# Kernel optimization log

Hardware: AMD Instinct MI355X
Metric: run time of the kernel (lower is better)

The kernel has to match this reference:

```python
import jax, jax.numpy as jnp
import numpy as np

N = 100000       # n nodes
NFEAT = 128
NHID1 = 128
NHID2 = 64
NCLASS = 8
E = 1_600_000    # edges per graph (avg degree 16)
HATT = 16        # Attention hidden_size default


def _glorot(k, shape):
    lim = jnp.sqrt(6.0 / (shape[0] + shape[1]))
    return jax.random.uniform(k, shape, minval=-lim, maxval=lim, dtype=jnp.float32)


def setup_inputs() -> dict:
    key = jax.random.key(0)
    ks = jax.random.split(key, 32)
    inp = {}
    inp["x"] = jax.random.normal(ks[0], (N, NFEAT), dtype=jnp.float32)
    inp["sadj_row"] = jax.random.randint(ks[1], (E,), 0, N)
    inp["sadj_col"] = jax.random.randint(ks[2], (E,), 0, N)
    inp["sadj_val"] = jax.random.uniform(ks[3], (E,), dtype=jnp.float32) / 16.0
    inp["fadj_row"] = jax.random.randint(ks[4], (E,), 0, N)
    inp["fadj_col"] = jax.random.randint(ks[5], (E,), 0, N)
    inp["fadj_val"] = jax.random.uniform(ks[6], (E,), dtype=jnp.float32) / 16.0
    # GCN weights: gc1 (nfeat->nhid1), gc2 (nhid1->nhid2), each with bias
    names = ["s1", "s2", "c"]
    for i, nm in enumerate(names):
        inp[f"w_{nm}_1"] = _glorot(ks[7 + 4 * i], (NFEAT, NHID1))
        inp[f"b_{nm}_1"] = jnp.zeros((NHID1,), jnp.float32)
        inp[f"w_{nm}_2"] = _glorot(ks[8 + 4 * i], (NHID1, NHID2))
        inp[f"b_{nm}_2"] = jnp.zeros((NHID2,), jnp.float32)
    # Attention: Linear(nhid2, 16) + Tanh + Linear(16, 1, bias=False)
    inp["att_w1"] = _glorot(ks[20], (NHID2, HATT))
    inp["att_b1"] = jnp.zeros((HATT,), jnp.float32)
    inp["att_w2"] = _glorot(ks[21], (HATT, 1))
    # MLP: Linear(nhid2, nclass)
    inp["mlp_w"] = _glorot(ks[22], (NHID2, NCLASS))
    inp["mlp_b"] = jnp.zeros((NCLASS,), jnp.float32)
    return inp


def _spmm(row, col, val, h):
    # (sparse adj) @ h : out[i] = sum_{edges (i,j)} val * h[j]
    return jax.ops.segment_sum(val[:, None] * h[col], row, num_segments=N)


def _gcn(x, row, col, val, w1, b1, w2, b2):
    h = jax.nn.relu(_spmm(row, col, val, x @ w1) + b1)  # dropout is identity (eval)
    return _spmm(row, col, val, h @ w2) + b2


def reference(x, sadj_row, sadj_col, sadj_val, fadj_row, fadj_col, fadj_val,
              w_s1_1, b_s1_1, w_s1_2, b_s1_2,
              w_s2_1, b_s2_1, w_s2_2, b_s2_2,
              w_c_1, b_c_1, w_c_2, b_c_2,
              att_w1, att_b1, att_w2, mlp_w, mlp_b):
    emb1 = _gcn(x, sadj_row, sadj_col, sadj_val, w_s1_1, b_s1_1, w_s1_2, b_s1_2)
    com1 = _gcn(x, sadj_row, sadj_col, sadj_val, w_c_1, b_c_1, w_c_2, b_c_2)
    com2 = _gcn(x, fadj_row, fadj_col, fadj_val, w_c_1, b_c_1, w_c_2, b_c_2)
    emb2 = _gcn(x, fadj_row, fadj_col, fadj_val, w_s2_1, b_s2_1, w_s2_2, b_s2_2)
    xcom = (com1 + com2) * 0.5
    z = jnp.stack([emb1, emb2, xcom], axis=1)          # [N, 3, nhid2]
    w = jnp.tanh(z @ att_w1 + att_b1) @ att_w2          # [N, 3, 1]
    beta = jax.nn.softmax(w, axis=1)
    emb = (beta * z).sum(axis=1)                        # [N, nhid2]
    output = jax.nn.log_softmax(emb @ mlp_w + mlp_b, axis=1)
    return (output, beta, emb1, com1, com2, emb2, emb)
```

## Files before the change

### kernel.cpp

```cpp
#include <hip/hip_runtime.h>


typedef unsigned short ushort_t;
typedef float f32x4 __attribute__((ext_vector_type(4)));
typedef short short8 __attribute__((ext_vector_type(8)));

#define NBLK1 512

__device__ __forceinline__ ushort_t f2bf(float f) {
  unsigned u = __float_as_uint(f);
  unsigned r = (u + 0x7FFFu + ((u >> 16) & 1u)) >> 16;
  return (ushort_t)r;
}
__device__ __forceinline__ float bf2f(ushort_t b) {
  return __uint_as_float((unsigned)b << 16);
}

__device__ __forceinline__ float rs16(const float a[16], int lane) {
  bool b8 = (lane & 8) != 0;
  float t[8];
#pragma unroll
  for (int j = 0; j < 8; ++j) {
    float sent = b8 ? a[j] : a[j + 8];
    float mine = b8 ? a[j + 8] : a[j];
    t[j] = mine + __shfl_xor(sent, 8);
  }
  bool b4 = (lane & 4) != 0;
  float u[4];
#pragma unroll
  for (int j = 0; j < 4; ++j) {
    float sent = b4 ? t[j] : t[j + 4];
    float mine = b4 ? t[j + 4] : t[j];
    u[j] = mine + __shfl_xor(sent, 4);
  }
  bool b2 = (lane & 2) != 0;
  float v[2];
#pragma unroll
  for (int j = 0; j < 2; ++j) {
    float s2 = b2 ? u[j] : u[j + 2];
    float m2 = b2 ? u[j + 2] : u[j];
    v[j] = m2 + __shfl_xor(s2, 2);
  }
  bool b1 = (lane & 1) != 0;
  float s1 = b1 ? v[0] : v[1];
  float m1 = b1 ? v[1] : v[0];
  return m1 + __shfl_xor(s1, 1);
}

__global__ __launch_bounds__(256) void cvt_bf16(
    const float* __restrict__ in, ushort_t* __restrict__ out, long total4) {
  long i = (long)blockIdx.x * 256 + threadIdx.x;
  if (i >= total4) return;
  float4 v = ((const float4*)in)[i];
  ushort4 o;
  o.x = f2bf(v.x);
  o.y = f2bf(v.y);
  o.z = f2bf(v.z);
  o.w = f2bf(v.w);
  ((ushort4*)out)[i] = o;
}

__global__ __launch_bounds__(256) void prep_weights(
    const float* __restrict__ w1a, const float* __restrict__ w1b,
    const float* __restrict__ w1c, const float* __restrict__ w2a,
    const float* __restrict__ w2b, const float* __restrict__ w2c,
    ushort_t* __restrict__ o1a, ushort_t* __restrict__ o1b,
    ushort_t* __restrict__ o1c, ushort_t* __restrict__ o2a,
    ushort_t* __restrict__ o2b, ushort_t* __restrict__ o2c) {
  int i = blockIdx.x * 256 + threadIdx.x;
  if (i < 49152) {
    int a = i >> 14, j = i & 16383;
    int nn = j >> 7, k = j & 127;
    const float* s = (a == 0) ? w1a : (a == 1) ? w1b : w1c;
    ushort_t* d = (a == 0) ? o1a : (a == 1) ? o1b : o1c;
    d[j] = f2bf(s[k * 128 + nn]);
  } else if (i < 73728) {
    int i2 = i - 49152;
    int a = i2 >> 13, j = i2 & 8191;
    int h = j >> 7, k = j & 127;
    const float* s = (a == 0) ? w2a : (a == 1) ? w2b : w2c;
    ushort_t* d = (a == 0) ? o2a : (a == 1) ? o2b : o2c;
    d[j] = f2bf(s[k * 64 + h]);
  }
}


__global__ __launch_bounds__(256) void coarse_hist(
    const int* __restrict__ rowS, const int* __restrict__ rowF,
    int* __restrict__ bkt_cnt, int n, int e, int nb) {
  __shared__ int lh[800];
  int t = threadIdx.x;
  for (int j = t; j < nb; j += 256) lh[j] = 0;
  __syncthreads();
  long total = 2L * e;
  long stride = (long)NBLK1 * 256;
  for (long i = (long)blockIdx.x * 256 + t; i < total; i += stride) {
    int vrow = (i < e) ? rowS[i] : (n + rowF[i - e]);
    atomicAdd(&lh[vrow >> 8], 1);
  }
  __syncthreads();
  for (int j = t; j < nb; j += 256)
    if (lh[j]) atomicAdd(&bkt_cnt[j], lh[j]);
}

__global__ __launch_bounds__(256) void coarse_scan(
    const int* __restrict__ cnt, int* __restrict__ off, int nb, int total) {
  __shared__ int lds[256];
  int t = threadIdx.x;
  int c[4];
  int s = 0;
#pragma unroll
  for (int j = 0; j < 4; ++j) {
    int idx = t * 4 + j;
    c[j] = (idx < nb) ? cnt[idx] : 0;
    s += c[j];
  }
  lds[t] = s;
  __syncthreads();
#pragma unroll
  for (int d = 1; d < 256; d <<= 1) {
    int v = (t >= d) ? lds[t - d] : 0;
    __syncthreads();
    lds[t] += v;
    __syncthreads();
  }
  int o = (t == 0) ? 0 : lds[t - 1];
#pragma unroll
  for (int j = 0; j < 4; ++j) {
    int idx = t * 4 + j;
    if (idx < nb) off[idx] = o;
    o += c[j];
  }
  if (t == 0) off[nb] = total;
}

__global__ __launch_bounds__(256) void coarse_scatter(
    const int* __restrict__ rowS, const int* __restrict__ colS,
    const float* __restrict__ valS, const int* __restrict__ rowF,
    const int* __restrict__ colF, const float* __restrict__ valF,
    const int* __restrict__ bkt_off, int* __restrict__ bkt_woff,
    int2* __restrict__ tmp, int n, int e, int nb) {
  __shared__ int lh[800];
  __shared__ int lb[800];
  __shared__ int gb[800];
  int t = threadIdx.x;
  for (int j = t; j < nb; j += 256) {
    lh[j] = 0;
    lb[j] = 0;
  }
  __syncthreads();
  long total = 2L * e;
  long stride = (long)NBLK1 * 256;
  for (long i = (long)blockIdx.x * 256 + t; i < total; i += stride) {
    int vrow = (i < e) ? rowS[i] : (n + rowF[i - e]);
    atomicAdd(&lh[vrow >> 8], 1);
  }
  __syncthreads();
  for (int j = t; j < nb; j += 256) {
    int h = lh[j];
    gb[j] = h ? (bkt_off[j] + atomicAdd(&bkt_woff[j], h)) : 0;
  }
  __syncthreads();
  for (long i = (long)blockIdx.x * 256 + t; i < total; i += stride) {
    int vrow, c;
    float v;
    if (i < e) {
      vrow = rowS[i];
      c = colS[i];
      v = valS[i];
    } else {
      vrow = n + rowF[i - e];
      c = colF[i - e];
      v = valF[i - e];
    }
    int b = vrow >> 8;
    int k = atomicAdd(&lb[b], 1);
    tmp[gb[b] + k] = make_int2(c | ((vrow & 255) << 24), __float_as_int(v));
  }
}

__global__ __launch_bounds__(256) void fine_sort(
    const int* __restrict__ bkt_off, const int2* __restrict__ tmp,
    int2* __restrict__ packed, int* __restrict__ rowptr, int vtotal,
    int etotal) {
  __shared__ int hist[256];
  __shared__ int scn[256];
  __shared__ int rowb[256];
  __shared__ int bump[256];
  int b = blockIdx.x;
  int t = threadIdx.x;
  int lo = bkt_off[b], hi = bkt_off[b + 1];
  hist[t] = 0;
  bump[t] = 0;
  __syncthreads();
  for (int i = lo + t; i < hi; i += 256)
    atomicAdd(&hist[((unsigned)tmp[i].x) >> 24], 1);
  __syncthreads();
  scn[t] = hist[t];
  __syncthreads();
#pragma unroll
  for (int d = 1; d < 256; d <<= 1) {
    int v = (t >= d) ? scn[t - d] : 0;
    __syncthreads();
    scn[t] += v;
    __syncthreads();
  }
  int rb = lo + ((t == 0) ? 0 : scn[t - 1]);
  rowb[t] = rb;
  int vrow = b * 256 + t;
  if (vrow < vtotal) rowptr[vrow] = rb;
  __syncthreads();
  for (int i = lo + t; i < hi; i += 256) {
    int2 p = tmp[i];
    int vl = ((unsigned)p.x) >> 24;
    int dest = rowb[vl] + atomicAdd(&bump[vl], 1);
    packed[dest] = make_int2(p.x & 0xFFFFFF, p.y);
  }
  if (b == 0 && t == 0) rowptr[vtotal] = etotal;
}


__global__ __launch_bounds__(256) void spmm_csr_128(
    const int* __restrict__ rowptr, const int2* __restrict__ packed,
    const ushort_t* __restrict__ h, ushort_t* __restrict__ Ax, int n) {
  int tid = threadIdx.x;
  int r = blockIdx.x * 8 + (tid >> 5);
  if (r >= n) return;
  int lane = tid & 31;
  int lo = rowptr[r], hi = rowptr[r + 1];
  const ushort4* h4 = (const ushort4*)h;
  float4 acc = make_float4(0.f, 0.f, 0.f, 0.f);
  int e = lo;
  for (; e + 4 <= hi; e += 4) {
    int2 p0 = packed[e], p1 = packed[e + 1], p2 = packed[e + 2],
         p3 = packed[e + 3];
    float v0 = __int_as_float(p0.y), v1 = __int_as_float(p1.y),
          v2 = __int_as_float(p2.y), v3 = __int_as_float(p3.y);
    ushort4 q0 = h4[(long)p0.x * 32 + lane];
    ushort4 q1 = h4[(long)p1.x * 32 + lane];
    ushort4 q2 = h4[(long)p2.x * 32 + lane];
    ushort4 q3 = h4[(long)p3.x * 32 + lane];
    acc.x += v0 * bf2f(q0.x) + v1 * bf2f(q1.x) + v2 * bf2f(q2.x) + v3 * bf2f(q3.x);
    acc.y += v0 * bf2f(q0.y) + v1 * bf2f(q1.y) + v2 * bf2f(q2.y) + v3 * bf2f(q3.y);
    acc.z += v0 * bf2f(q0.z) + v1 * bf2f(q1.z) + v2 * bf2f(q2.z) + v3 * bf2f(q3.z);
    acc.w += v0 * bf2f(q0.w) + v1 * bf2f(q1.w) + v2 * bf2f(q2.w) + v3 * bf2f(q3.w);
  }
  for (; e < hi; ++e) {
    int2 p = packed[e];
    float v = __int_as_float(p.y);
    ushort4 q = h4[(long)p.x * 32 + lane];
    acc.x += v * bf2f(q.x);
    acc.y += v * bf2f(q.y);
    acc.z += v * bf2f(q.z);
    acc.w += v * bf2f(q.w);
  }
  ushort4 o;
  o.x = f2bf(acc.x);
  o.y = f2bf(acc.y);
  o.z = f2bf(acc.z);
  o.w = f2bf(acc.w);
  ((ushort4*)Ax)[(long)r * 32 + lane] = o;
}

__global__ __launch_bounds__(256) void spmm_dual64(
    const int* __restrict__ rowptr, const int2* __restrict__ packed,
    const ushort_t* __restrict__ hS, const ushort_t* __restrict__ hC,
    const float* __restrict__ bS, const float* __restrict__ bC,
    float* __restrict__ outS, float* __restrict__ outC, int n) {
  int tid = threadIdx.x;
  int r = blockIdx.x * 8 + (tid >> 5);
  if (r >= n) return;
  int lane = tid & 31;
  int half = lane >> 4;
  int li = lane & 15;
  const ushort4* h4 = (const ushort4*)(half ? hC : hS);
  float4 acc = ((const float4*)(half ? bC : bS))[li];
  int lo = rowptr[r], hi = rowptr[r + 1];
  int e = lo;
  for (; e + 4 <= hi; e += 4) {
    int2 p0 = packed[e], p1 = packed[e + 1], p2 = packed[e + 2],
         p3 = packed[e + 3];
    float v0 = __int_as_float(p0.y), v1 = __int_as_float(p1.y),
          v2 = __int_as_float(p2.y), v3 = __int_as_float(p3.y);
    ushort4 q0 = h4[(long)p0.x * 16 + li];
    ushort4 q1 = h4[(long)p1.x * 16 + li];
    ushort4 q2 = h4[(long)p2.x * 16 + li];
    ushort4 q3 = h4[(long)p3.x * 16 + li];
    acc.x += v0 * bf2f(q0.x) + v1 * bf2f(q1.x) + v2 * bf2f(q2.x) + v3 * bf2f(q3.x);
    acc.y += v0 * bf2f(q0.y) + v1 * bf2f(q1.y) + v2 * bf2f(q2.y) + v3 * bf2f(q3.y);
    acc.z += v0 * bf2f(q0.z) + v1 * bf2f(q1.z) + v2 * bf2f(q2.z) + v3 * bf2f(q3.z);
    acc.w += v0 * bf2f(q0.w) + v1 * bf2f(q1.w) + v2 * bf2f(q2.w) + v3 * bf2f(q3.w);
  }
  for (; e < hi; ++e) {
    int2 p = packed[e];
    float v = __int_as_float(p.y);
    ushort4 q = h4[(long)p.x * 16 + li];
    acc.x += v * bf2f(q.x);
    acc.y += v * bf2f(q.y);
    acc.z += v * bf2f(q.z);
    acc.w += v * bf2f(q.w);
  }
  float4* o = (float4*)(half ? outC : outS);
  o[(long)r * 16 + li] = acc;
}

__device__ __forceinline__ void l1l2_chain(
    const ushort_t* __restrict__ Ax, const ushort_t* __restrict__ W1T,
    const float* __restrict__ B1, const ushort_t* __restrict__ W2T,
    ushort_t* __restrict__ H, int n, long node0, int w, int lo16, int g,
    ushort_t (*sp)[136]) {
  f32x4 acc1[2][4];
#pragma unroll
  for (int m = 0; m < 2; ++m)
#pragma unroll
    for (int nu = 0; nu < 4; ++nu) acc1[m][nu] = (f32x4){0.f, 0.f, 0.f, 0.f};

#pragma unroll 1
  for (int t = 0; t < 4; ++t) {
    short8 af0 = *(const short8*)(W1T + (32 * w + lo16) * 128 + 32 * t + 8 * g);
    short8 af1 =
        *(const short8*)(W1T + (32 * w + 16 + lo16) * 128 + 32 * t + 8 * g);
#pragma unroll
    for (int nu = 0; nu < 4; ++nu) {
      long node = node0 + 16 * nu + lo16;
      if (node > (long)n - 1) node = (long)n - 1;
      short8 bf = *(const short8*)(Ax + node * 128 + 32 * t + 8 * g);
      acc1[0][nu] =
          __builtin_amdgcn_mfma_f32_16x16x32_bf16(af0, bf, acc1[0][nu], 0, 0, 0);
      acc1[1][nu] =
          __builtin_amdgcn_mfma_f32_16x16x32_bf16(af1, bf, acc1[1][nu], 0, 0, 0);
    }
  }

#pragma unroll
  for (int m = 0; m < 2; ++m) {
    int sf = 32 * w + 16 * m + 4 * g;
    float4 b1v = *(const float4*)(B1 + sf);
#pragma unroll
    for (int nu = 0; nu < 4; ++nu) {
      int node_l = 16 * nu + lo16;
      ushort4 pk;
      pk.x = f2bf(fmaxf(acc1[m][nu][0] + b1v.x, 0.f));
      pk.y = f2bf(fmaxf(acc1[m][nu][1] + b1v.y, 0.f));
      pk.z = f2bf(fmaxf(acc1[m][nu][2] + b1v.z, 0.f));
      pk.w = f2bf(fmaxf(acc1[m][nu][3] + b1v.w, 0.f));
      *(ushort4*)(&sp[node_l][sf]) = pk;
    }
  }
  __syncthreads();

  f32x4 acc2[4];
#pragma unroll
  for (int nu = 0; nu < 4; ++nu) acc2[nu] = (f32x4){0.f, 0.f, 0.f, 0.f};
#pragma unroll 1
  for (int t = 0; t < 4; ++t) {
    short8 af = *(const short8*)(&sp[16 * w + lo16][32 * t + 8 * g]);
#pragma unroll
    for (int nu = 0; nu < 4; ++nu) {
      short8 bf =
          *(const short8*)(W2T + (16 * nu + lo16) * 128 + 32 * t + 8 * g);
      acc2[nu] =
          __builtin_amdgcn_mfma_f32_16x16x32_bf16(af, bf, acc2[nu], 0, 0, 0);
    }
  }
#pragma unroll
  for (int nu = 0; nu < 4; ++nu) {
#pragma unroll
    for (int r = 0; r < 4; ++r) {
      long node = node0 + 16 * w + 4 * g + r;
      if (node < n) H[node * 64 + 16 * nu + lo16] = f2bf(acc2[nu][r]);
    }
  }
}

__global__ __launch_bounds__(256) void fused_l1l2_mfma_dual(
    const ushort_t* __restrict__ Ax, const ushort_t* __restrict__ W1Ta,
    const float* __restrict__ B1a, const ushort_t* __restrict__ W2Ta,
    ushort_t* __restrict__ Ha, const ushort_t* __restrict__ W1Tb,
    const float* __restrict__ B1b, const ushort_t* __restrict__ W2Tb,
    ushort_t* __restrict__ Hb, int n) {
  __shared__ __attribute__((aligned(16))) ushort_t sp[64][136];
  int tid = threadIdx.x;
  int w = tid >> 6;
  int l = tid & 63;
  int lo16 = l & 15;
  int g = l >> 4;
  long node0 = (long)blockIdx.x * 64;

  l1l2_chain(Ax, W1Ta, B1a, W2Ta, Ha, n, node0, w, lo16, g, sp);
  __syncthreads();
  l1l2_chain(Ax, W1Tb, B1b, W2Tb, Hb, n, node0, w, lo16, g, sp);
}

__global__ __launch_bounds__(256) void final_fuse(
    const float* __restrict__ emb1, const float* __restrict__ emb2,
    const float* __restrict__ com1, const float* __restrict__ com2,
    const float* __restrict__ attw1, const float* __restrict__ attb1,
    const float* __restrict__ attw2, const float* __restrict__ mlpw,
    const float* __restrict__ mlpb, float* __restrict__ out_logp,
    float* __restrict__ out_beta, float* __restrict__ out_emb, int n) {
  __shared__ __attribute__((aligned(16))) float w1t[16][64];
  __shared__ __attribute__((aligned(16))) float mwt[8][64];
  __shared__ float b1s[16];
  __shared__ float w2s[16];
  __shared__ float mbs[8];
  int tid = threadIdx.x;
  for (int idx = tid; idx < 1024; idx += 256)
    w1t[idx & 15][idx >> 4] = attw1[idx];
  for (int idx = tid; idx < 512; idx += 256)
    mwt[idx & 7][idx >> 3] = mlpw[idx];
  if (tid < 16) {
    b1s[tid] = attb1[tid];
    w2s[tid] = attw2[tid];
  }
  if (tid < 8) mbs[tid] = mlpb[tid];
  __syncthreads();

  int lane = tid & 15;
  long i = ((long)blockIdx.x * 256 + tid) >> 4;
  bool alive = i < n;
  long ii = alive ? i : (long)(n - 1);

  float4 z0 = ((const float4*)emb1)[ii * 16 + lane];
  float4 z1 = ((const float4*)emb2)[ii * 16 + lane];
  float4 x1 = ((const float4*)com1)[ii * 16 + lane];
  float4 x2 = ((const float4*)com2)[ii * 16 + lane];
  float4 z2 = make_float4(0.5f * (x1.x + x2.x), 0.5f * (x1.y + x2.y),
                          0.5f * (x1.z + x2.z), 0.5f * (x1.w + x2.w));

  float a0[16], a1[16], a2[16];
#pragma unroll
  for (int m = 0; m < 16; ++m) {
    float4 w = *(const float4*)&w1t[m][lane * 4];
    a0[m] = z0.x * w.x + z0.y * w.y + z0.z * w.z + z0.w * w.w;
    a1[m] = z1.x * w.x + z1.y * w.y + z1.z * w.z + z1.w * w.w;
    a2[m] = z2.x * w.x + z2.y * w.y + z2.z * w.z + z2.w * w.w;
  }
  float A0 = rs16(a0, lane);
  float A1 = rs16(a1, lane);
  float A2 = rs16(a2, lane);
  float bm = b1s[lane], wm = w2s[lane];
  float p0 = tanhf(A0 + bm) * wm;
  float p1 = tanhf(A1 + bm) * wm;
  float p2 = tanhf(A2 + bm) * wm;
#pragma unroll
  for (int d = 1; d < 16; d <<= 1) {
    p0 += __shfl_xor(p0, d);
    p1 += __shfl_xor(p1, d);
    p2 += __shfl_xor(p2, d);
  }
  float mx = fmaxf(p0, fmaxf(p1, p2));
  float ex0 = expf(p0 - mx), ex1 = expf(p1 - mx), ex2 = expf(p2 - mx);
  float inv = 1.f / (ex0 + ex1 + ex2);
  float be0 = ex0 * inv, be1 = ex1 * inv, be2 = ex2 * inv;

  float4 em;
  em.x = be0 * z0.x + be1 * z1.x + be2 * z2.x;
  em.y = be0 * z0.y + be1 * z1.y + be2 * z2.y;
  em.z = be0 * z0.z + be1 * z1.z + be2 * z2.z;
  em.w = be0 * z0.w + be1 * z1.w + be2 * z2.w;
  if (alive) ((float4*)out_emb)[i * 16 + lane] = em;

  float lg[8];
#pragma unroll
  for (int p = 0; p < 8; ++p) {
    float4 w = *(const float4*)&mwt[p][lane * 4];
    lg[p] = em.x * w.x + em.y * w.y + em.z * w.z + em.w * w.w;
  }
  bool b8 = (lane & 8) != 0;
  float t4[4];
#pragma unroll
  for (int j = 0; j < 4; ++j) {
    float sent = b8 ? lg[j] : lg[j + 4];
    float mine = b8 ? lg[j + 4] : lg[j];
    t4[j] = mine + __shfl_xor(sent, 8);
  }
  bool b4 = (lane & 4) != 0;
  float t2[2];
#pragma unroll
  for (int j = 0; j < 2; ++j) {
    float sent = b4 ? t4[j] : t4[j + 2];
    float mine = b4 ? t4[j + 2] : t4[j];
    t2[j] = mine + __shfl_xor(sent, 4);
  }
  bool b2 = (lane & 2) != 0;
  {
    float sent = b2 ? t2[0] : t2[1];
    float mine = b2 ? t2[1] : t2[0];
    t2[0] = mine + __shfl_xor(sent, 2);
  }
  t2[0] += __shfl_xor(t2[0], 1);
  int myidx = (b8 ? 4 : 0) + (b4 ? 2 : 0) + (b2 ? 1 : 0);
  float lgv = t2[0] + mbs[myidx];
  float m2 = lgv;
  m2 = fmaxf(m2, __shfl_xor(m2, 2));
  m2 = fmaxf(m2, __shfl_xor(m2, 4));
  m2 = fmaxf(m2, __shfl_xor(m2, 8));
  float ev = expf(lgv - m2);
  float ssum = ev;
  ssum += __shfl_xor(ssum, 2);
  ssum += __shfl_xor(ssum, 4);
  ssum += __shfl_xor(ssum, 8);
  float ls = m2 + logf(ssum);

  if (alive) {
    if ((lane & 1) == 0) out_logp[i * 8 + myidx] = lgv - ls;
    if (lane == 0) {
      out_beta[i * 3 + 0] = be0;
      out_beta[i * 3 + 1] = be1;
      out_beta[i * 3 + 2] = be2;
    }
  }
}

extern "C" void kernel_launch(void* const* d_in, const int* in_sizes, int n_in,
                              void* d_out, int out_size, void* d_ws,
                              size_t ws_size, hipStream_t stream) {
  const float* x = (const float*)d_in[0];
  const int* srow = (const int*)d_in[1];
  const int* scol_in = (const int*)d_in[2];
  const float* sval_in = (const float*)d_in[3];
  const int* frow = (const int*)d_in[4];
  const int* fcol_in = (const int*)d_in[5];
  const float* fval_in = (const float*)d_in[6];
  const float* w_s1_1 = (const float*)d_in[7];
  const float* b_s1_1 = (const float*)d_in[8];
  const float* w_s1_2 = (const float*)d_in[9];
  const float* b_s1_2 = (const float*)d_in[10];
  const float* w_s2_1 = (const float*)d_in[11];
  const float* b_s2_1 = (const float*)d_in[12];
  const float* w_s2_2 = (const float*)d_in[13];
  const float* b_s2_2 = (const float*)d_in[14];
  const float* w_c_1 = (const float*)d_in[15];
  const float* b_c_1 = (const float*)d_in[16];
  const float* w_c_2 = (const float*)d_in[17];
  const float* b_c_2 = (const float*)d_in[18];
  const float* attw1 = (const float*)d_in[19];
  const float* attb1 = (const float*)d_in[20];
  const float* attw2 = (const float*)d_in[21];
  const float* mlpw = (const float*)d_in[22];
  const float* mlpb = (const float*)d_in[23];

  const int n = in_sizes[0] / 128;
  const int e = in_sizes[1];
  const int vtotal = 2 * n;
  const int nb = (vtotal + 255) >> 8;

  float* out = (float*)d_out;
  float* o_logp = out;
  float* o_beta = out + (size_t)n * 8;
  float* o_emb1 = out + (size_t)n * 11;
  float* o_com1 = o_emb1 + (size_t)n * 64;
  float* o_com2 = o_com1 + (size_t)n * 64;
  float* o_emb2 = o_com2 + (size_t)n * 64;
  float* o_emb = o_emb2 + (size_t)n * 64;

  ushort_t* x_bf16 = (ushort_t*)o_emb;
  int2* tmp = (int2*)o_emb1;

  ushort_t* ax = (ushort_t*)d_ws;
  ushort_t* hwS = ax + (size_t)n * 128;
  ushort_t* hwC = hwS + (size_t)n * 64;
  ushort_t* w1t_s1 = hwC + (size_t)n * 64;
  ushort_t* w1t_s2 = w1t_s1 + 16384;
  ushort_t* w1t_c = w1t_s2 + 16384;
  ushort_t* w2t_s1 = w1t_c + 16384;
  ushort_t* w2t_s2 = w2t_s1 + 8192;
  ushort_t* w2t_c = w2t_s2 + 8192;
  int* rowptr = (int*)(w2t_c + 8192);
  int* bkt_cnt = rowptr + vtotal + 1;
  int* bkt_woff = bkt_cnt + nb;
  int* bkt_off = bkt_woff + nb;
  int* tail = bkt_off + nb + 2;
  int2* packed = (int2*)(tail + ((((size_t)(tail)&7) == 0) ? 0 : 1));

  const int spmmBlocks = (n + 7) / 8;
  const int cvtBlocks = (int)(((long)n * 32 + 255) / 256);
  const int mfmaBlocks = (n + 63) / 64;

  cvt_bf16<<<cvtBlocks, 256, 0, stream>>>(x, x_bf16, (long)n * 32);
  prep_weights<<<288, 256, 0, stream>>>(w_s1_1, w_s2_1, w_c_1, w_s1_2, w_s2_2,
                                        w_c_2, w1t_s1, w1t_s2, w1t_c, w2t_s1,
                                        w2t_s2, w2t_c);

  hipMemsetAsync(bkt_cnt, 0, (size_t)(2 * nb) * sizeof(int), stream);
  coarse_hist<<<NBLK1, 256, 0, stream>>>(srow, frow, bkt_cnt, n, e, nb);
  coarse_scan<<<1, 256, 0, stream>>>(bkt_cnt, bkt_off, nb, 2 * e);
  coarse_scatter<<<NBLK1, 256, 0, stream>>>(srow, scol_in, sval_in, frow,
                                            fcol_in, fval_in, bkt_off,
                                            bkt_woff, tmp, n, e, nb);
  fine_sort<<<nb, 256, 0, stream>>>(bkt_off, tmp, packed, rowptr, vtotal,
                                    2 * e);

  const int* rowptrS = rowptr;
  const int* rowptrF = rowptr + n;

  spmm_csr_128<<<spmmBlocks, 256, 0, stream>>>(rowptrS, packed, x_bf16, ax, n);
  fused_l1l2_mfma_dual<<<mfmaBlocks, 256, 0, stream>>>(
      ax, w1t_s1, b_s1_1, w2t_s1, hwS, w1t_c, b_c_1, w2t_c, hwC, n);
  spmm_dual64<<<spmmBlocks, 256, 0, stream>>>(rowptrS, packed, hwS, hwC,
                                              b_s1_2, b_c_2, o_emb1, o_com1,
                                              n);

  spmm_csr_128<<<spmmBlocks, 256, 0, stream>>>(rowptrF, packed, x_bf16, ax, n);
  fused_l1l2_mfma_dual<<<mfmaBlocks, 256, 0, stream>>>(
      ax, w1t_s2, b_s2_1, w2t_s2, hwS, w1t_c, b_c_1, w2t_c, hwC, n);
  spmm_dual64<<<spmmBlocks, 256, 0, stream>>>(rowptrF, packed, hwS, hwC,
                                              b_s2_2, b_c_2, o_emb2, o_com2,
                                              n);

  final_fuse<<<(int)(((long)n * 16 + 255) / 256), 256, 0, stream>>>(
      o_emb1, o_emb2, o_com1, o_com2, attw1, attb1, attw2, mlpw, mlpb, o_logp,
      o_beta, o_emb, n);
}
```

Measured before the change: 581.3 us.

## Interleave hidden outputs per node and widen sort buckets to 512 rows

The two layer-2 hidden matrices (specific and common branches) are now written into one interleaved buffer of 128 bf16 per node. Each 64-wide gather in the dual SpMM then becomes one contiguous 256-byte row read instead of two separate 128-byte reads. The coarse bucket sort switches from 256-row to 512-row buckets and doubles the scatter grid, which halves the bucket count and the fine-sort block count. Column indices are now packed into 20 bits with 9 bits of local row, which still holds because N=100000 fits in 2^20.

```diff
diff --git a/kernel.cpp b/kernel.cpp
--- a/kernel.cpp
+++ b/kernel.cpp
@@ -5,7 +5,9 @@
 typedef float f32x4 __attribute__((ext_vector_type(4)));
 typedef short short8 __attribute__((ext_vector_type(8)));
 
-#define NBLK1 512
+#define NBLK1 1024
+#define BKT_BITS 9
+#define BKT_ROWS 512
 
 __device__ __forceinline__ ushort_t f2bf(float f) {
   unsigned u = __float_as_uint(f);
@@ -88,7 +90,7 @@
 __global__ __launch_bounds__(256) void coarse_hist(
     const int* __restrict__ rowS, const int* __restrict__ rowF,
     int* __restrict__ bkt_cnt, int n, int e, int nb) {
-  __shared__ int lh[800];
+  __shared__ int lh[400];
   int t = threadIdx.x;
   for (int j = t; j < nb; j += 256) lh[j] = 0;
   __syncthreads();
@@ -96,7 +98,7 @@
   long stride = (long)NBLK1 * 256;
   for (long i = (long)blockIdx.x * 256 + t; i < total; i += stride) {
     int vrow = (i < e) ? rowS[i] : (n + rowF[i - e]);
-    atomicAdd(&lh[vrow >> 8], 1);
+    atomicAdd(&lh[vrow >> BKT_BITS], 1);
   }
   __syncthreads();
   for (int j = t; j < nb; j += 256)
@@ -140,9 +142,9 @@
     const int* __restrict__ colF, const float* __restrict__ valF,
     const int* __restrict__ bkt_off, int* __restrict__ bkt_woff,
     int2* __restrict__ tmp, int n, int e, int nb) {
-  __shared__ int lh[800];
-  __shared__ int lb[800];
-  __shared__ int gb[800];
+  __shared__ int lh[400];
+  __shared__ int lb[400];
+  __shared__ int gb[400];
   int t = threadIdx.x;
   for (int j = t; j < nb; j += 256) {
     lh[j] = 0;
@@ -153,7 +155,7 @@
   long stride = (long)NBLK1 * 256;
   for (long i = (long)blockIdx.x * 256 + t; i < total; i += stride) {
     int vrow = (i < e) ? rowS[i] : (n + rowF[i - e]);
-    atomicAdd(&lh[vrow >> 8], 1);
+    atomicAdd(&lh[vrow >> BKT_BITS], 1);
   }
   __syncthreads();
   for (int j = t; j < nb; j += 256) {
@@ -173,9 +175,10 @@
       c = colF[i - e];
       v = valF[i - e];
     }
-    int b = vrow >> 8;
+    int b = vrow >> BKT_BITS;
     int k = atomicAdd(&lb[b], 1);
-    tmp[gb[b] + k] = make_int2(c | ((vrow & 255) << 24), __float_as_int(v));
+    tmp[gb[b] + k] =
+        make_int2(c | ((vrow & (BKT_ROWS - 1)) << 20), __float_as_int(v));
   }
 }
 
@@ -183,20 +186,23 @@
     const int* __restrict__ bkt_off, const int2* __restrict__ tmp,
     int2* __restrict__ packed, int* __restrict__ rowptr, int vtotal,
     int etotal) {
-  __shared__ int hist[256];
+  __shared__ int hist[512];
   __shared__ int scn[256];
-  __shared__ int rowb[256];
-  __shared__ int bump[256];
+  __shared__ int rowb[512];
+  __shared__ int bump[512];
   int b = blockIdx.x;
   int t = threadIdx.x;
   int lo = bkt_off[b], hi = bkt_off[b + 1];
   hist[t] = 0;
+  hist[t + 256] = 0;
   bump[t] = 0;
+  bump[t + 256] = 0;
   __syncthreads();
   for (int i = lo + t; i < hi; i += 256)
-    atomicAdd(&hist[((unsigned)tmp[i].x) >> 24], 1);
-  __syncthreads();
-  scn[t] = hist[t];
+    atomicAdd(&hist[((unsigned)tmp[i].x) >> 20], 1);
+  __syncthreads();
+  int s = hist[2 * t] + hist[2 * t + 1];
+  scn[t] = s;
   __syncthreads();
 #pragma unroll
   for (int d = 1; d < 256; d <<= 1) {
@@ -205,16 +211,20 @@
     scn[t] += v;
     __syncthreads();
   }
-  int rb = lo + ((t == 0) ? 0 : scn[t - 1]);
-  rowb[t] = rb;
-  int vrow = b * 256 + t;
-  if (vrow < vtotal) rowptr[vrow] = rb;
+  int pre = (t == 0) ? 0 : scn[t - 1];
+  int r0 = lo + pre;
+  int r1 = r0 + hist[2 * t];
+  rowb[2 * t] = r0;
+  rowb[2 * t + 1] = r1;
+  int vrow0 = b * BKT_ROWS + 2 * t;
+  if (vrow0 < vtotal) rowptr[vrow0] = r0;
+  if (vrow0 + 1 < vtotal) rowptr[vrow0 + 1] = r1;
   __syncthreads();
   for (int i = lo + t; i < hi; i += 256) {
     int2 p = tmp[i];
-    int vl = ((unsigned)p.x) >> 24;
+    int vl = ((unsigned)p.x) >> 20;
     int dest = rowb[vl] + atomicAdd(&bump[vl], 1);
-    packed[dest] = make_int2(p.x & 0xFFFFFF, p.y);
+    packed[dest] = make_int2(p.x & 0xFFFFF, p.y);
   }
   if (b == 0 && t == 0) rowptr[vtotal] = etotal;
 }
@@ -264,16 +274,16 @@
 
 __global__ __launch_bounds__(256) void spmm_dual64(
     const int* __restrict__ rowptr, const int2* __restrict__ packed,
-    const ushort_t* __restrict__ hS, const ushort_t* __restrict__ hC,
-    const float* __restrict__ bS, const float* __restrict__ bC,
-    float* __restrict__ outS, float* __restrict__ outC, int n) {
+    const ushort_t* __restrict__ hI, const float* __restrict__ bS,
+    const float* __restrict__ bC, float* __restrict__ outS,
+    float* __restrict__ outC, int n) {
   int tid = threadIdx.x;
   int r = blockIdx.x * 8 + (tid >> 5);
   if (r >= n) return;
   int lane = tid & 31;
   int half = lane >> 4;
   int li = lane & 15;
-  const ushort4* h4 = (const ushort4*)(half ? hC : hS);
+  const ushort4* h4 = (const ushort4*)hI;
   float4 acc = ((const float4*)(half ? bC : bS))[li];
   int lo = rowptr[r], hi = rowptr[r + 1];
   int e = lo;
@@ -282,10 +292,10 @@
          p3 = packed[e + 3];
     float v0 = __int_as_float(p0.y), v1 = __int_as_float(p1.y),
           v2 = __int_as_float(p2.y), v3 = __int_as_float(p3.y);
-    ushort4 q0 = h4[(long)p0.x * 16 + li];
-    ushort4 q1 = h4[(long)p1.x * 16 + li];
-    ushort4 q2 = h4[(long)p2.x * 16 + li];
-    ushort4 q3 = h4[(long)p3.x * 16 + li];
+    ushort4 q0 = h4[(long)p0.x * 32 + lane];
+    ushort4 q1 = h4[(long)p1.x * 32 + lane];
+    ushort4 q2 = h4[(long)p2.x * 32 + lane];
+    ushort4 q3 = h4[(long)p3.x * 32 + lane];
     acc.x += v0 * bf2f(q0.x) + v1 * bf2f(q1.x) + v2 * bf2f(q2.x) + v3 * bf2f(q3.x);
     acc.y += v0 * bf2f(q0.y) + v1 * bf2f(q1.y) + v2 * bf2f(q2.y) + v3 * bf2f(q3.y);
     acc.z += v0 * bf2f(q0.z) + v1 * bf2f(q1.z) + v2 * bf2f(q2.z) + v3 * bf2f(q3.z);
@@ -294,7 +304,7 @@
   for (; e < hi; ++e) {
     int2 p = packed[e];
     float v = __int_as_float(p.y);
-    ushort4 q = h4[(long)p.x * 16 + li];
+    ushort4 q = h4[(long)p.x * 32 + lane];
     acc.x += v * bf2f(q.x);
     acc.y += v * bf2f(q.y);
     acc.z += v * bf2f(q.z);
@@ -307,8 +317,8 @@
 __device__ __forceinline__ void l1l2_chain(
     const ushort_t* __restrict__ Ax, const ushort_t* __restrict__ W1T,
     const float* __restrict__ B1, const ushort_t* __restrict__ W2T,
-    ushort_t* __restrict__ H, int n, long node0, int w, int lo16, int g,
-    ushort_t (*sp)[136]) {
+    ushort_t* __restrict__ HI, int hoff, int n, long node0, int w, int lo16,
+    int g, ushort_t (*sp)[136]) {
   f32x4 acc1[2][4];
 #pragma unroll
   for (int m = 0; m < 2; ++m)
@@ -368,7 +378,7 @@
 #pragma unroll
     for (int r = 0; r < 4; ++r) {
       long node = node0 + 16 * w + 4 * g + r;
-      if (node < n) H[node * 64 + 16 * nu + lo16] = f2bf(acc2[nu][r]);
+      if (node < n) HI[node * 128 + hoff + 16 * nu + lo16] = f2bf(acc2[nu][r]);
     }
   }
 }
@@ -376,9 +386,8 @@
 __global__ __launch_bounds__(256) void fused_l1l2_mfma_dual(
     const ushort_t* __restrict__ Ax, const ushort_t* __restrict__ W1Ta,
     const float* __restrict__ B1a, const ushort_t* __restrict__ W2Ta,
-    ushort_t* __restrict__ Ha, const ushort_t* __restrict__ W1Tb,
-    const float* __restrict__ B1b, const ushort_t* __restrict__ W2Tb,
-    ushort_t* __restrict__ Hb, int n) {
+    const ushort_t* __restrict__ W1Tb, const float* __restrict__ B1b,
+    const ushort_t* __restrict__ W2Tb, ushort_t* __restrict__ HI, int n) {
   __shared__ __attribute__((aligned(16))) ushort_t sp[64][136];
   int tid = threadIdx.x;
   int w = tid >> 6;
@@ -387,9 +396,9 @@
   int g = l >> 4;
   long node0 = (long)blockIdx.x * 64;
 
-  l1l2_chain(Ax, W1Ta, B1a, W2Ta, Ha, n, node0, w, lo16, g, sp);
-  __syncthreads();
-  l1l2_chain(Ax, W1Tb, B1b, W2Tb, Hb, n, node0, w, lo16, g, sp);
+  l1l2_chain(Ax, W1Ta, B1a, W2Ta, HI, 0, n, node0, w, lo16, g, sp);
+  __syncthreads();
+  l1l2_chain(Ax, W1Tb, B1b, W2Tb, HI, 64, n, node0, w, lo16, g, sp);
 }
 
 __global__ __launch_bounds__(256) void final_fuse(
@@ -544,7 +553,7 @@
   const int n = in_sizes[0] / 128;
   const int e = in_sizes[1];
   const int vtotal = 2 * n;
-  const int nb = (vtotal + 255) >> 8;
+  const int nb = (vtotal + BKT_ROWS - 1) >> BKT_BITS;
 
   float* out = (float*)d_out;
   float* o_logp = out;
@@ -559,9 +568,8 @@
   int2* tmp = (int2*)o_emb1;
 
   ushort_t* ax = (ushort_t*)d_ws;
-  ushort_t* hwS = ax + (size_t)n * 128;
-  ushort_t* hwC = hwS + (size_t)n * 64;
-  ushort_t* w1t_s1 = hwC + (size_t)n * 64;
+  ushort_t* hwI = ax + (size_t)n * 128;
+  ushort_t* w1t_s1 = hwI + (size_t)n * 128;
   ushort_t* w1t_s2 = w1t_s1 + 16384;
   ushort_t* w1t_c = w1t_s2 + 16384;
   ushort_t* w2t_s1 = w1t_c + 16384;
@@ -597,17 +605,15 @@
 
   spmm_csr_128<<<spmmBlocks, 256, 0, stream>>>(rowptrS, packed, x_bf16, ax, n);
   fused_l1l2_mfma_dual<<<mfmaBlocks, 256, 0, stream>>>(
-      ax, w1t_s1, b_s1_1, w2t_s1, hwS, w1t_c, b_c_1, w2t_c, hwC, n);
-  spmm_dual64<<<spmmBlocks, 256, 0, stream>>>(rowptrS, packed, hwS, hwC,
-                                              b_s1_2, b_c_2, o_emb1, o_com1,
-                                              n);
+      ax, w1t_s1, b_s1_1, w2t_s1, w1t_c, b_c_1, w2t_c, hwI, n);
+  spmm_dual64<<<spmmBlocks, 256, 0, stream>>>(rowptrS, packed, hwI, b_s1_2,
+                                              b_c_2, o_emb1, o_com1, n);
 
   spmm_csr_128<<<spmmBlocks, 256, 0, stream>>>(rowptrF, packed, x_bf16, ax, n);
   fused_l1l2_mfma_dual<<<mfmaBlocks, 256, 0, stream>>>(
-      ax, w1t_s2, b_s2_1, w2t_s2, hwS, w1t_c, b_c_1, w2t_c, hwC, n);
-  spmm_dual64<<<spmmBlocks, 256, 0, stream>>>(rowptrF, packed, hwS, hwC,
-                                              b_s2_2, b_c_2, o_emb2, o_com2,
-                                              n);
+      ax, w1t_s2, b_s2_1, w2t_s2, w1t_c, b_c_1, w2t_c, hwI, n);
+  spmm_dual64<<<spmmBlocks, 256, 0, stream>>>(rowptrF, packed, hwI, b_s2_2,
+                                              b_c_2, o_emb2, o_com2, n);
 
   final_fuse<<<(int)(((long)n * 16 + 255) / 256), 256, 0, stream>>>(
       o_emb1, o_emb2, o_com1, o_com2, attw1, attb1, attw2, mlpw, mlpb, o_logp,
```

After: 602.0 us. 1.04x slower.
